# Optimization experiments

Measured on AMD Instinct MI355X. Metric: run time of the kernel, lower is better.

The kernel has to match this reference:

```python
import jax, jax.numpy as jnp
from jax import lax
import numpy as np

H = 48; W = 48; C_IN = 256; A_PER = 3
M = A_PER * H * W            # 6912 anchors
IMG = 768.0                  # square image, clip bound for x and y
OBJ_THR = 0.3; IOU_THR = 0.7; TOP_K = 2000
NEG = -1e9                   # finite sentinel for masked scores


def _make_anchors():
    stride = IMG / H
    base = 2.0 * stride
    ratios = np.array([0.5, 1.0, 2.0])
    ws = base * np.sqrt(ratios)          # [3]
    hs = base / np.sqrt(ratios)
    cx = (np.arange(W) + 0.5) * stride
    cy = (np.arange(H) + 0.5) * stride
    cxg, cyg = np.meshgrid(cx, cy)       # [H, W]
    anc = np.stack([
        cxg[None] - ws[:, None, None] / 2,
        cyg[None] - hs[:, None, None] / 2,
        cxg[None] + ws[:, None, None] / 2,
        cyg[None] + hs[:, None, None] / 2,
    ], axis=-1)                           # [3, H, W, 4] matches (anchor, h, w) flatten order
    return jnp.asarray(anc.reshape(-1, 4), jnp.float32)


def setup_inputs() -> dict:
    key = jax.random.key(0)
    ks = jax.random.split(key, 4)
    x = jax.random.normal(ks[0], (1, C_IN, H, W), jnp.float32)
    conv_w = jax.random.normal(ks[1], (256, 256, 3, 3), jnp.float32) * 0.02
    conv_b = jnp.zeros((256,), jnp.float32)
    det_w = jax.random.normal(ks[2], (3, 256, 1, 1), jnp.float32) * 0.02
    det_b = jnp.zeros((3,), jnp.float32)
    reg_w = jax.random.normal(ks[3], (12, 256, 1, 1), jnp.float32) * 0.02
    reg_b = jnp.zeros((12,), jnp.float32)
    anchors = _make_anchors()
    return {"x": x, "conv_w": conv_w, "conv_b": conv_b, "det_w": det_w,
            "det_b": det_b, "reg_w": reg_w, "reg_b": reg_b, "anchors": anchors}


def reference(x, conv_w, conv_b, det_w, det_b, reg_w, reg_b, anchors):
    # ---- FPN 3x3 conv + RPN head (1x1 convs) ----
    inter = lax.conv_general_dilated(
        x, conv_w, (1, 1), 'SAME',
        dimension_numbers=('NCHW', 'OIHW', 'NCHW')) + conv_b[None, :, None, None]
    obj = jax.nn.sigmoid(jnp.einsum('nchw,oc->nohw', inter, det_w[:, :, 0, 0])
                         + det_b[None, :, None, None])          # [1,3,H,W]
    reg = (jnp.einsum('nchw,oc->nohw', inter, reg_w[:, :, 0, 0])
           + reg_b[None, :, None, None])                        # [1,12,H,W]

    scores = obj.reshape(-1)                                    # [M], (anchor,h,w) order
    deltas = reg.reshape(1, 4, A_PER, H, W).transpose(0, 2, 3, 4, 1).reshape(-1, 4)

    # ---- box decode (preserves the source's cx/cy quirk: cx = y1 + w/2, cy = x1 + h/2) ----
    x1, y1, x2, y2 = anchors[:, 0], anchors[:, 1], anchors[:, 2], anchors[:, 3]
    aw = x2 - x1; ah = y2 - y1
    acx = y1 + aw / 2; acy = x1 + ah / 2
    dx, dy, dw, dh = deltas[:, 0], deltas[:, 1], deltas[:, 2], deltas[:, 3]
    px = acx + dx * aw; py = acy + dy * ah
    pw = aw * jnp.exp(dw); ph = ah * jnp.exp(dh)
    boxes = jnp.stack([px - pw / 2, py - ph / 2, px + pw / 2, py + ph / 2], axis=-1)

    # ---- clip to image ----
    boxes = jnp.clip(boxes, 0.0, IMG)

    # ---- validity: degenerate filter (source's naming quirk) + objectness threshold ----
    hts = boxes[:, 2] - boxes[:, 0]
    wds = boxes[:, 3] - boxes[:, 1]
    valid = (hts > 0) & (wds > 0) & (scores > OBJ_THR)

    # ---- greedy NMS (jit-friendly: sort, pairwise IoU, sequential suppression) ----
    s = jnp.where(valid, scores, NEG)
    order = jnp.argsort(-s)
    b = boxes[order]; v = valid[order]; ss = s[order]
    area = (b[:, 2] - b[:, 0]) * (b[:, 3] - b[:, 1])             # [M]
    iw = jnp.clip(jnp.minimum(b[:, None, 2], b[None, :, 2])
                  - jnp.maximum(b[:, None, 0], b[None, :, 0]), 0.0)
    ih = jnp.clip(jnp.minimum(b[:, None, 3], b[None, :, 3])
                  - jnp.maximum(b[:, None, 1], b[None, :, 1]), 0.0)
    inter_a = iw * ih                                             # [M,M]
    iou = inter_a / jnp.maximum(area[:, None] + area[None, :] - inter_a, 1e-9)

    idx = jnp.arange(M)

    def body(suppressed, i):
        keep_i = v[i] & (~suppressed[i])
        sup = keep_i & (iou[i] > IOU_THR) & (idx > i)
        return suppressed | sup, keep_i

    _, keeps = lax.scan(body, jnp.zeros(M, bool), idx)            # keep mask (sorted order)

    # ---- top-k proposal selection (fixed K, padded with sentinels) ----
    out_s = jnp.where(keeps, ss, NEG)
    topv, topi = lax.top_k(out_s, TOP_K)
    vtop = keeps[topi]
    out_scores = jnp.where(vtop, topv, -1.0)                      # [TOP_K]
    out_boxes = jnp.where(vtop[:, None], b[topi], 0.0)            # [TOP_K, 4]
    return out_scores, out_boxes
```

## Files before the change

kernel.cpp:

```cpp
#include <hip/hip_runtime.h>
#include <cstdint>

#define NPX 2304
#define MM 6912
#define NW 108
#define TOPK 2000
#define NEGV -1000000000.0f
#define OBJ_THRF 0.3f
#define IOU_THRF 0.7f
#define IMGF 768.0f
#define KSPLIT 8

typedef unsigned long long u64;
typedef unsigned int u32;

__device__ __forceinline__ u64 shfl64(u64 v, int src) {
  int lo = __shfl((int)(v & 0xffffffffull), src, 64);
  int hi = __shfl((int)(v >> 32), src, 64);
  return ((u64)(u32)hi << 32) | (u32)lo;
}

__global__ __launch_bounds__(256) void k_wt(const float* __restrict__ cw,
                                            float* __restrict__ wt) {
  __shared__ float t[64][65];
  const int it0 = blockIdx.x * 64;
  const int oc0 = blockIdx.y * 64;
  const int tx = threadIdx.x & 63;
  const int ty = threadIdx.x >> 6;
#pragma unroll
  for (int k = 0; k < 16; ++k) {
    int oc = ty + k * 4;
    t[oc][tx] = cw[(oc0 + oc) * 2304 + it0 + tx];
  }
  __syncthreads();
#pragma unroll
  for (int k = 0; k < 16; ++k) {
    int it = ty + k * 4;
    wt[(it0 + it) * 256 + oc0 + tx] = t[tx][it];
  }
}

__global__ __launch_bounds__(256) void k_conv(const float* __restrict__ x,
                                              const float* __restrict__ wt,
                                              float* __restrict__ part) {
  __shared__ float xs[16 * 8 * 52];
  const int tid = threadIdx.x;
  const int px = blockIdx.x * 256 + tid;
  const int oc0 = blockIdx.y * 16;
  const int ks = blockIdx.z;
  const int row = px / 48, col = px % 48;
  const int r0 = (blockIdx.x * 256) / 48;
  const int rbase = row - r0;

  float st[25];
#pragma unroll
  for (int k = 0; k < 25; ++k) {
    int e = tid + k * 256;
    int ic = e / 400, rem = e % 400;
    int r = rem / 50, c = rem % 50 - 1;
    int gr = r0 - 1 + r;
    float v = 0.f;
    if (c >= 0 && c < 48 && gr >= 0 && gr < 48)
      v = x[(ks * 32 + ic) * NPX + gr * 48 + c];
    st[k] = v;
  }

  float acc[16];
#pragma unroll
  for (int k = 0; k < 16; ++k) acc[k] = 0.f;

  for (int icc = 0; icc < 2; ++icc) {
    __builtin_amdgcn_sched_barrier(0);
    __builtin_amdgcn_s_barrier();
    __builtin_amdgcn_sched_barrier(0);
#pragma unroll
    for (int k = 0; k < 25; ++k) {
      int e = tid + k * 256;
      int ic = e / 400, rem = e % 400;
      int r = rem / 50, c = rem % 50;
      xs[(ic * 8 + r) * 52 + c] = st[k];
    }
    if (icc == 0) {
#pragma unroll
      for (int k = 0; k < 25; ++k) {
        int e = tid + k * 256;
        int ic = e / 400, rem = e % 400;
        int r = rem / 50, c = rem % 50 - 1;
        int gr = r0 - 1 + r;
        float v = 0.f;
        if (c >= 0 && c < 48 && gr >= 0 && gr < 48)
          v = x[(ks * 32 + 16 + ic) * NPX + gr * 48 + c];
        st[k] = v;
      }
    }
    asm volatile("s_waitcnt lgkmcnt(0)" ::: "memory");
    __builtin_amdgcn_s_barrier();
    __builtin_amdgcn_sched_barrier(0);
    const int icg0 = ks * 32 + icc * 16;
    for (int ic = 0; ic < 16; ++ic) {
      float xv[9];
#pragma unroll
      for (int dr = 0; dr < 3; ++dr)
#pragma unroll
        for (int dc = 0; dc < 3; ++dc)
          xv[dr * 3 + dc] = xs[(ic * 8 + rbase + dr) * 52 + col + dc];
      const float* wrow = wt + (size_t)(icg0 + ic) * 9 * 256 + oc0;
#pragma unroll
      for (int t = 0; t < 9; ++t) {
        const float* wp = wrow + t * 256;
#pragma unroll
        for (int k = 0; k < 16; ++k) acc[k] += xv[t] * wp[k];
      }
    }
  }
#pragma unroll
  for (int k = 0; k < 16; ++k)
    part[((size_t)ks * 256 + oc0 + k) * NPX + px] = acc[k];
}

__global__ __launch_bounds__(64) void k_dq(const float* __restrict__ part,
                                           const float* __restrict__ cb,
                                           const float* __restrict__ dw,
                                           const float* __restrict__ rw,
                                           float* __restrict__ qacc) {
  __shared__ float wl[64 * 16];
  const int tid = threadIdx.x;
  const int cq = blockIdx.y;
  const int px = blockIdx.x * 64 + tid;
  for (int e = tid; e < 960; e += 64) {
    int o = e % 15, ci = e / 15;
    int c = cq * 64 + ci;
    wl[ci * 16 + o] = (o < 3) ? dw[o * 256 + c] : rw[(o - 3) * 256 + c];
  }
  __syncthreads();
  float acc[15];
#pragma unroll
  for (int o = 0; o < 15; o++) acc[o] = 0.f;
#pragma unroll 4
  for (int ci = 0; ci < 64; ++ci) {
    int c = cq * 64 + ci;
    float v = cb[c];
#pragma unroll
    for (int kks = 0; kks < KSPLIT; ++kks)
      v += part[((size_t)kks * 256 + c) * NPX + px];
#pragma unroll
    for (int o = 0; o < 15; o++) acc[o] += v * wl[ci * 16 + o];
  }
#pragma unroll
  for (int o = 0; o < 15; o++)
    qacc[((size_t)cq * NPX + px) * 16 + o] = acc[o];
}

__global__ __launch_bounds__(64) void k_dfin(const float* __restrict__ qacc,
                                             const float* __restrict__ db,
                                             const float* __restrict__ rb,
                                             const float* __restrict__ anch,
                                             float* __restrict__ s,
                                             float4* __restrict__ boxes) {
  const int tid = threadIdx.x;
  const int p = blockIdx.x * 64 + tid;
  float a[15];
#pragma unroll
  for (int o = 0; o < 15; o++)
    a[o] = qacc[((size_t)0 * NPX + p) * 16 + o] +
           qacc[((size_t)1 * NPX + p) * 16 + o] +
           qacc[((size_t)2 * NPX + p) * 16 + o] +
           qacc[((size_t)3 * NPX + p) * 16 + o];
  const float4* an4 = (const float4*)anch;
#pragma unroll
  for (int aa = 0; aa < 3; ++aa) {
    int m = aa * NPX + p;
    float logit = a[aa] + db[aa];
    float score = 1.f / (1.f + expf(-logit));
    float dxv = a[3 + 0 + aa] + rb[0 + aa];
    float dyv = a[3 + 3 + aa] + rb[3 + aa];
    float dwv = a[3 + 6 + aa] + rb[6 + aa];
    float dhv = a[3 + 9 + aa] + rb[9 + aa];
    float4 an = an4[m];
    float aw = an.z - an.x;
    float ah = an.w - an.y;
    float acx = an.y + aw * 0.5f;
    float acy = an.x + ah * 0.5f;
    float pxc = acx + dxv * aw;
    float pyc = acy + dyv * ah;
    float pw = aw * expf(dwv);
    float ph = ah * expf(dhv);
    float b0 = pxc - pw * 0.5f, b1 = pyc - ph * 0.5f;
    float b2 = pxc + pw * 0.5f, b3 = pyc + ph * 0.5f;
    b0 = fminf(fmaxf(b0, 0.f), IMGF);
    b1 = fminf(fmaxf(b1, 0.f), IMGF);
    b2 = fminf(fmaxf(b2, 0.f), IMGF);
    b3 = fminf(fmaxf(b3, 0.f), IMGF);
    float hts = b2 - b0, wds = b3 - b1;
    bool valid = (hts > 0.f) && (wds > 0.f) && (score > OBJ_THRF);
    s[m] = valid ? score : NEGV;
    boxes[m] = make_float4(b0, b1, b2, b3);
  }
}

__global__ __launch_bounds__(256) void k_sortA(const float* __restrict__ s,
                                               u64* __restrict__ keys) {
  __shared__ u64 lds[1024];
  const int tid = threadIdx.x;
  const int b = blockIdx.x;
  for (int v = tid; v < 1024; v += 256) {
    int i = b * 1024 + v;
    u64 p;
    if (i < MM) {
      u32 u = __float_as_uint(s[i]);
      u = u ^ (u32)(((int)u >> 31) | 0x80000000);
      p = ((u64)(~u) << 32) | (u32)i;
    } else {
      p = ~0ull;
    }
    lds[v] = p;
  }
  for (u32 kk = 2; kk <= 1024; kk <<= 1) {
    for (u32 j = kk >> 1; j > 0; j >>= 1) {
      __syncthreads();
#pragma unroll 2
      for (int t = tid; t < 512; t += 256) {
        int i = ((t & ~(j - 1)) << 1) | (t & (j - 1));
        int l = i | j;
        bool up = ((i & kk) == 0);
        u64 a = lds[i], c = lds[l];
        u64 mn = a < c ? a : c;
        u64 mx = a < c ? c : a;
        lds[i] = up ? mn : mx;
        lds[l] = up ? mx : mn;
      }
    }
  }
  __syncthreads();
  for (int v = tid; v < 1024; v += 256) keys[b * 1024 + v] = lds[v];
}

__global__ __launch_bounds__(256) void k_merge(const u64* __restrict__ in,
                                               u64* __restrict__ outk, int L, int fin,
                                               const float* __restrict__ s,
                                               const float4* __restrict__ boxes,
                                               float* __restrict__ ssc,
                                               float4* __restrict__ sboxes) {
  const int i = blockIdx.x * 256 + threadIdx.x;
  const int pair = i / (2 * L);
  const int r = i - pair * 2 * L;
  const u64* A = in + (size_t)pair * 2 * L;
  const u64* B = A + L;
  int lo = (r > L) ? (r - L) : 0;
  int hi = (r < L) ? r : L;
  while (lo < hi) {
    int mid = (lo + hi) >> 1;
    if (A[mid] < B[r - 1 - mid]) lo = mid + 1; else hi = mid;
  }
  int a = lo, bi = r - lo;
  u64 av = (a < L) ? A[a] : ~0ull;
  u64 bv = (bi < L) ? B[bi] : ~0ull;
  u64 o = (av < bv) ? av : bv;
  outk[i] = o;
  if (fin && i < MM) {
    int idx = (int)(u32)o;
    ssc[i] = s[idx];
    sboxes[i] = boxes[idx];
  }
}

__global__ __launch_bounds__(256) void k_zero(u64* __restrict__ nz) {
  int i = blockIdx.x * 256 + threadIdx.x;
  if (i < MM * 2) nz[i] = 0;
}

__global__ __launch_bounds__(256) void k_mask(const float4* __restrict__ sboxes,
                                              u64* __restrict__ mask_t,
                                              u64* __restrict__ nz) {
  __shared__ float4 rb_[64];
  const int rt = blockIdx.x;
  const int w = blockIdx.y * 4 + (threadIdx.x >> 6);
  const int lane = threadIdx.x & 63;
  if (threadIdx.x < 64) rb_[threadIdx.x] = sboxes[rt * 64 + threadIdx.x];
  __syncthreads();
  if (w < rt) return;
  float4 c = sboxes[w * 64 + lane];
  float areaC = (c.z - c.x) * (c.w - c.y);
  u64 myw = 0;
  for (int r = 0; r < 64; ++r) {
    float4 b = rb_[r];
    float iw = fmaxf(fminf(b.z, c.z) - fmaxf(b.x, c.x), 0.f);
    float ih = fmaxf(fminf(b.w, c.w) - fmaxf(b.y, c.y), 0.f);
    float inter = iw * ih;
    float areaB = (b.z - b.x) * (b.w - b.y);
    float un = fmaxf(areaB + areaC - inter, 1e-9f);
    bool bit = (inter / un) > IOU_THRF;
    u64 bal = __ballot(bit);
    if (lane == r) myw = bal;
  }
  mask_t[(size_t)w * MM + rt * 64 + lane] = myw;
  if (myw) atomicOr(&nz[(rt * 64 + lane) * 2 + (w >> 6)], 1ull << (w & 63));
}

__global__ __launch_bounds__(256) void k_scan(const u64* __restrict__ mask_t,
                                              const u64* __restrict__ nz,
                                              const float* __restrict__ ssc,
                                              const float4* __restrict__ sboxes,
                                              float* __restrict__ out) {
  __shared__ u64 remv[NW];
  __shared__ u64 keepw[NW];
  __shared__ int blist[64];
  __shared__ int nkS;
  __shared__ int kcntS;
  __shared__ int pref[NW];
  const int tid = threadIdx.x;
  if (tid < NW) { remv[tid] = 0; keepw[tid] = 0; }
  if (tid == 0) kcntS = 0;
  __syncthreads();

  for (int c = 0; c < NW; ++c) {
    if (tid < 64) {
      const int lane = tid;
      u64 dg = mask_t[(size_t)c * MM + c * 64 + lane];
      float sv = ssc[c * 64 + lane];
      u64 vb = __ballot(sv > OBJ_THRF);
      u64 w0 = remv[c];
      u64 cand = vb & ~w0;
      u64 above = (lane < 63) ? ~((2ull << lane) - 1ull) : 0ull;
      bool inC = ((cand >> lane) & 1ull) != 0;
      u64 conf = __ballot(inC && ((dg & above & cand) != 0ull));
      u64 kb;
      if (conf == 0ull) {
        kb = cand;
      } else {
        u64 w = w0;
        kb = 0;
        u64 rem = cand;
        while (rem) {
          int b = __ffsll(rem) - 1;
          kb |= (1ull << b);
          w |= shfl64(dg, b);
          rem = vb & ~w;
        }
      }
      int below = __popcll(kb & ((1ull << lane) - 1ull));
      if ((kb >> lane) & 1ull) blist[below] = lane;
      if (lane == 0) {
        keepw[c] = kb;
        nkS = __popcll(kb);
        kcntS += __popcll(kb);
      }
    }
    __syncthreads();
    int nk = nkS;
    if (tid < nk) {
      int row = c * 64 + blist[tid];
      u64 nz0 = nz[row * 2], nz1 = nz[row * 2 + 1];
      if (c < 64) {
        nz0 &= (c < 63) ? ~((2ull << c) - 1ull) : 0ull;
      } else {
        nz0 = 0;
        int cc = c - 64;
        nz1 &= ~((2ull << cc) - 1ull);
      }
      while (nz0) {
        int wv = __ffsll(nz0) - 1; nz0 &= nz0 - 1;
        atomicOr(&remv[wv], mask_t[(size_t)wv * MM + row]);
      }
      while (nz1) {
        int wv = __ffsll(nz1) - 1; nz1 &= nz1 - 1;
        atomicOr(&remv[wv + 64], mask_t[(size_t)(wv + 64) * MM + row]);
      }
    }
    __syncthreads();
    if (kcntS >= TOPK) break;
  }

  if (tid == 0) {
    int run = 0;
    for (int cc = 0; cc < NW; ++cc) { pref[cc] = run; run += __popcll(keepw[cc]); }
  }
  __syncthreads();
  for (int e = tid; e < TOPK * 5; e += 256) out[e] = (e < TOPK) ? -1.0f : 0.0f;
  __syncthreads();
  float4* ob = (float4*)(out + TOPK);
  for (int i = tid; i < MM; i += 256) {
    int cc = i >> 6, b = i & 63;
    u64 kb = keepw[cc];
    if ((kb >> b) & 1ull) {
      int rank = pref[cc] + __popcll(kb & ((1ull << b) - 1ull));
      if (rank < TOPK) {
        out[rank] = ssc[i];
        ob[rank] = sboxes[i];
      }
    }
  }
}

extern "C" void kernel_launch(void* const* d_in, const int* in_sizes, int n_in,
                              void* d_out, int out_size, void* d_ws, size_t ws_size,
                              hipStream_t stream) {
  const float* x  = (const float*)d_in[0];
  const float* cw = (const float*)d_in[1];
  const float* cb = (const float*)d_in[2];
  const float* dw = (const float*)d_in[3];
  const float* db = (const float*)d_in[4];
  const float* rw = (const float*)d_in[5];
  const float* rb = (const float*)d_in[6];
  const float* an = (const float*)d_in[7];
  char* ws = (char*)d_ws;
  float*  part   = (float*)(ws);
  u64*    keysA  = (u64*)(ws);
  u64*    keysB  = (u64*)(ws + 65536);
  u64*    mask   = (u64*)(ws);
  u64*    nz     = (u64*)(ws + 5971968);
  float*  wt     = (float*)(ws + 18874368);
  float*  qacc   = (float*)(ws + 18874368);
  float*  s      = (float*)(ws + 21233664);
  float4* boxes  = (float4*)(ws + 21261312);
  float*  ssc    = (float*)(ws + 21371904);
  float4* sboxes = (float4*)(ws + 21399552);
  float* out = (float*)d_out;

  hipLaunchKernelGGL(k_wt, dim3(36, 4), dim3(256), 0, stream, cw, wt);
  hipLaunchKernelGGL(k_conv, dim3(9, 16, KSPLIT), dim3(256), 0, stream, x, wt, part);
  hipLaunchKernelGGL(k_dq, dim3(36, 4), dim3(64), 0, stream, part, cb, dw, rw, qacc);
  hipLaunchKernelGGL(k_dfin, dim3(36), dim3(64), 0, stream, qacc, db, rb, an, s, boxes);
  hipLaunchKernelGGL(k_zero, dim3(54), dim3(256), 0, stream, nz);
  hipLaunchKernelGGL(k_sortA, dim3(8), dim3(256), 0, stream, s, keysA);
  hipLaunchKernelGGL(k_merge, dim3(32), dim3(256), 0, stream, keysA, keysB, 1024, 0, s, boxes, ssc, sboxes);
  hipLaunchKernelGGL(k_merge, dim3(32), dim3(256), 0, stream, keysB, keysA, 2048, 0, s, boxes, ssc, sboxes);
  hipLaunchKernelGGL(k_merge, dim3(32), dim3(256), 0, stream, keysA, keysB, 4096, 1, s, boxes, ssc, sboxes);
  hipLaunchKernelGGL(k_mask, dim3(108, 27), dim3(256), 0, stream, sboxes, mask, nz);
  hipLaunchKernelGGL(k_scan, dim3(1), dim3(256), 0, stream, mask, nz, ssc, sboxes, out);
}
```

Before: 323.8 us.

## Use direct global-to-LDS loads in conv, split reduction, fold zeroing, cache scan data in LDS

The conv kernel now stages both input-channel halves straight into double-buffered LDS with global_load_lds instead of routing them through registers. The k-split partial sum moves out of k_dq into a new wide k_red kernel, so k_dq reads a reduced intermediate. The nz zeroing is folded into k_sortA, removing one launch. The serial NMS scan preloads the diagonal mask words and sorted scores into LDS to avoid global loads in its loop. Risks: the global_load_lds destination address math (e & ~63 with per-lane offset) must match the padded 50-wide layout. The extra k_red pass also adds a full read and write of the intermediate.

```diff
diff --git a/kernel.cpp b/kernel.cpp
--- a/kernel.cpp
+++ b/kernel.cpp
@@ -20,6 +20,12 @@
   return ((u64)(u32)hi << 32) | (u32)lo;
 }
 
+__device__ __forceinline__ void gl_lds(const float* g, float* l) {
+  __builtin_amdgcn_global_load_lds(
+      (const __attribute__((address_space(1))) void*)g,
+      (__attribute__((address_space(3))) void*)l, 4, 0, 0);
+}
+
 __global__ __launch_bounds__(256) void k_wt(const float* __restrict__ cw,
                                             float* __restrict__ wt) {
   __shared__ float t[64][65];
@@ -43,7 +49,7 @@
 __global__ __launch_bounds__(256) void k_conv(const float* __restrict__ x,
                                               const float* __restrict__ wt,
                                               float* __restrict__ part) {
-  __shared__ float xs[16 * 8 * 52];
+  __shared__ float xs[2][16 * 8 * 50];
   const int tid = threadIdx.x;
   const int px = blockIdx.x * 256 + tid;
   const int oc0 = blockIdx.y * 16;
@@ -52,50 +58,42 @@
   const int r0 = (blockIdx.x * 256) / 48;
   const int rbase = row - r0;
 
-  float st[25];
+  {
+    float4 z4 = make_float4(0.f, 0.f, 0.f, 0.f);
+    float4* p4 = (float4*)&xs[0][0];
+    for (int e = tid; e < 2 * 6400 / 4; e += 256) p4[e] = z4;
+  }
+  __syncthreads();
+
+  float acc[16];
+#pragma unroll
+  for (int k = 0; k < 16; ++k) acc[k] = 0.f;
+
 #pragma unroll
   for (int k = 0; k < 25; ++k) {
     int e = tid + k * 256;
     int ic = e / 400, rem = e % 400;
-    int r = rem / 50, c = rem % 50 - 1;
-    int gr = r0 - 1 + r;
-    float v = 0.f;
-    if (c >= 0 && c < 48 && gr >= 0 && gr < 48)
-      v = x[(ks * 32 + ic) * NPX + gr * 48 + c];
-    st[k] = v;
-  }
-
-  float acc[16];
-#pragma unroll
-  for (int k = 0; k < 16; ++k) acc[k] = 0.f;
+    int r = rem / 50, c = rem % 50;
+    int gr = r0 - 1 + r, gc = c - 1;
+    if (gc >= 0 && gc < 48 && gr >= 0 && gr < 48)
+      gl_lds(x + (size_t)(ks * 32 + ic) * NPX + gr * 48 + gc,
+             &xs[0][e & ~63]);
+  }
+  __syncthreads();
+
+#pragma unroll
+  for (int k = 0; k < 25; ++k) {
+    int e = tid + k * 256;
+    int ic = e / 400, rem = e % 400;
+    int r = rem / 50, c = rem % 50;
+    int gr = r0 - 1 + r, gc = c - 1;
+    if (gc >= 0 && gc < 48 && gr >= 0 && gr < 48)
+      gl_lds(x + (size_t)(ks * 32 + 16 + ic) * NPX + gr * 48 + gc,
+             &xs[1][e & ~63]);
+  }
 
   for (int icc = 0; icc < 2; ++icc) {
-    __builtin_amdgcn_sched_barrier(0);
-    __builtin_amdgcn_s_barrier();
-    __builtin_amdgcn_sched_barrier(0);
-#pragma unroll
-    for (int k = 0; k < 25; ++k) {
-      int e = tid + k * 256;
-      int ic = e / 400, rem = e % 400;
-      int r = rem / 50, c = rem % 50;
-      xs[(ic * 8 + r) * 52 + c] = st[k];
-    }
-    if (icc == 0) {
-#pragma unroll
-      for (int k = 0; k < 25; ++k) {
-        int e = tid + k * 256;
-        int ic = e / 400, rem = e % 400;
-        int r = rem / 50, c = rem % 50 - 1;
-        int gr = r0 - 1 + r;
-        float v = 0.f;
-        if (c >= 0 && c < 48 && gr >= 0 && gr < 48)
-          v = x[(ks * 32 + 16 + ic) * NPX + gr * 48 + c];
-        st[k] = v;
-      }
-    }
-    asm volatile("s_waitcnt lgkmcnt(0)" ::: "memory");
-    __builtin_amdgcn_s_barrier();
-    __builtin_amdgcn_sched_barrier(0);
+    const float* xb = &xs[icc][0];
     const int icg0 = ks * 32 + icc * 16;
     for (int ic = 0; ic < 16; ++ic) {
       float xv[9];
@@ -103,7 +101,7 @@
       for (int dr = 0; dr < 3; ++dr)
 #pragma unroll
         for (int dc = 0; dc < 3; ++dc)
-          xv[dr * 3 + dc] = xs[(ic * 8 + rbase + dr) * 52 + col + dc];
+          xv[dr * 3 + dc] = xb[(ic * 8 + rbase + dr) * 50 + col + dc];
       const float* wrow = wt + (size_t)(icg0 + ic) * 9 * 256 + oc0;
 #pragma unroll
       for (int t = 0; t < 9; ++t) {
@@ -112,14 +110,26 @@
         for (int k = 0; k < 16; ++k) acc[k] += xv[t] * wp[k];
       }
     }
+    if (icc == 0) __syncthreads();
   }
 #pragma unroll
   for (int k = 0; k < 16; ++k)
     part[((size_t)ks * 256 + oc0 + k) * NPX + px] = acc[k];
 }
 
-__global__ __launch_bounds__(64) void k_dq(const float* __restrict__ part,
-                                           const float* __restrict__ cb,
+__global__ __launch_bounds__(256) void k_red(const float* __restrict__ part,
+                                             const float* __restrict__ cb,
+                                             float* __restrict__ inter) {
+  const int px = blockIdx.x * 256 + threadIdx.x;
+  const int c  = blockIdx.y;
+  float v = cb[c];
+#pragma unroll
+  for (int ks = 0; ks < KSPLIT; ++ks)
+    v += part[((size_t)ks * 256 + c) * NPX + px];
+  inter[(size_t)c * NPX + px] = v;
+}
+
+__global__ __launch_bounds__(64) void k_dq(const float* __restrict__ inter,
                                            const float* __restrict__ dw,
                                            const float* __restrict__ rw,
                                            float* __restrict__ qacc) {
@@ -139,10 +149,7 @@
 #pragma unroll 4
   for (int ci = 0; ci < 64; ++ci) {
     int c = cq * 64 + ci;
-    float v = cb[c];
-#pragma unroll
-    for (int kks = 0; kks < KSPLIT; ++kks)
-      v += part[((size_t)kks * 256 + c) * NPX + px];
+    float v = inter[(size_t)c * NPX + px];
 #pragma unroll
     for (int o = 0; o < 15; o++) acc[o] += v * wl[ci * 16 + o];
   }
@@ -199,10 +206,12 @@
 }
 
 __global__ __launch_bounds__(256) void k_sortA(const float* __restrict__ s,
-                                               u64* __restrict__ keys) {
+                                               u64* __restrict__ keys,
+                                               u64* __restrict__ nz) {
   __shared__ u64 lds[1024];
   const int tid = threadIdx.x;
   const int b = blockIdx.x;
+  for (int i = b * 256 + tid; i < MM * 2; i += 8 * 256) nz[i] = 0;
   for (int v = tid; v < 1024; v += 256) {
     int i = b * 1024 + v;
     u64 p;
@@ -264,11 +273,6 @@
   }
 }
 
-__global__ __launch_bounds__(256) void k_zero(u64* __restrict__ nz) {
-  int i = blockIdx.x * 256 + threadIdx.x;
-  if (i < MM * 2) nz[i] = 0;
-}
-
 __global__ __launch_bounds__(256) void k_mask(const float4* __restrict__ sboxes,
                                               u64* __restrict__ mask_t,
                                               u64* __restrict__ nz) {
@@ -302,6 +306,8 @@
                                               const float* __restrict__ ssc,
                                               const float4* __restrict__ sboxes,
                                               float* __restrict__ out) {
+  __shared__ u64 diagL[NW * 64];
+  __shared__ float sscL[MM];
   __shared__ u64 remv[NW];
   __shared__ u64 keepw[NW];
   __shared__ int blist[64];
@@ -309,6 +315,9 @@
   __shared__ int kcntS;
   __shared__ int pref[NW];
   const int tid = threadIdx.x;
+  for (int e = tid; e < NW * 64; e += 256)
+    diagL[e] = mask_t[(size_t)(e >> 6) * MM + (e >> 6) * 64 + (e & 63)];
+  for (int e = tid; e < MM; e += 256) sscL[e] = ssc[e];
   if (tid < NW) { remv[tid] = 0; keepw[tid] = 0; }
   if (tid == 0) kcntS = 0;
   __syncthreads();
@@ -316,8 +325,8 @@
   for (int c = 0; c < NW; ++c) {
     if (tid < 64) {
       const int lane = tid;
-      u64 dg = mask_t[(size_t)c * MM + c * 64 + lane];
-      float sv = ssc[c * 64 + lane];
+      u64 dg = diagL[c * 64 + lane];
+      float sv = sscL[c * 64 + lane];
       u64 vb = __ballot(sv > OBJ_THRF);
       u64 w0 = remv[c];
       u64 cand = vb & ~w0;
@@ -385,7 +394,7 @@
     if ((kb >> b) & 1ull) {
       int rank = pref[cc] + __popcll(kb & ((1ull << b) - 1ull));
       if (rank < TOPK) {
-        out[rank] = ssc[i];
+        out[rank] = sscL[i];
         ob[rank] = sboxes[i];
       }
     }
@@ -405,12 +414,13 @@
   const float* an = (const float*)d_in[7];
   char* ws = (char*)d_ws;
   float*  part   = (float*)(ws);
+  float*  qacc   = (float*)(ws);
   u64*    keysA  = (u64*)(ws);
   u64*    keysB  = (u64*)(ws + 65536);
   u64*    mask   = (u64*)(ws);
   u64*    nz     = (u64*)(ws + 5971968);
   float*  wt     = (float*)(ws + 18874368);
-  float*  qacc   = (float*)(ws + 18874368);
+  float*  inter  = (float*)(ws + 18874368);
   float*  s      = (float*)(ws + 21233664);
   float4* boxes  = (float4*)(ws + 21261312);
   float*  ssc    = (float*)(ws + 21371904);
@@ -419,10 +429,10 @@
 
   hipLaunchKernelGGL(k_wt, dim3(36, 4), dim3(256), 0, stream, cw, wt);
   hipLaunchKernelGGL(k_conv, dim3(9, 16, KSPLIT), dim3(256), 0, stream, x, wt, part);
-  hipLaunchKernelGGL(k_dq, dim3(36, 4), dim3(64), 0, stream, part, cb, dw, rw, qacc);
+  hipLaunchKernelGGL(k_red, dim3(9, 256), dim3(256), 0, stream, part, cb, inter);
+  hipLaunchKernelGGL(k_dq, dim3(36, 4), dim3(64), 0, stream, inter, dw, rw, qacc);
   hipLaunchKernelGGL(k_dfin, dim3(36), dim3(64), 0, stream, qacc, db, rb, an, s, boxes);
-  hipLaunchKernelGGL(k_zero, dim3(54), dim3(256), 0, stream, nz);
-  hipLaunchKernelGGL(k_sortA, dim3(8), dim3(256), 0, stream, s, keysA);
+  hipLaunchKernelGGL(k_sortA, dim3(8), dim3(256), 0, stream, s, keysA, nz);
   hipLaunchKernelGGL(k_merge, dim3(32), dim3(256), 0, stream, keysA, keysB, 1024, 0, s, boxes, ssc, sboxes);
   hipLaunchKernelGGL(k_merge, dim3(32), dim3(256), 0, stream, keysB, keysA, 2048, 0, s, boxes, ssc, sboxes);
   hipLaunchKernelGGL(k_merge, dim3(32), dim3(256), 0, stream, keysA, keysB, 4096, 1, s, boxes, ssc, sboxes);
```

After: 269.6 us. 1.2x faster.
